# Optimization experiments

Measured on AMD Instinct MI355X. Metric: run time of the kernel, lower is better.

## Reference

```python
import jax, jax.numpy as jnp
import numpy as np

DIM_V = 512
H = 8
EPS = 1e-5

def _layernorm(x, g, b):
    mu = jnp.mean(x, axis=-1, keepdims=True)
    var = jnp.var(x, axis=-1, keepdims=True)
    return (x - mu) * jax.lax.rsqrt(var + EPS) * g + b

def setup_inputs() -> dict:
    key = jax.random.key(0)
    ks = jax.random.split(key, 10)
    B, Nq, Nk, dq, dk, dv = 8, 1024, 1024, 512, 512, DIM_V
    def lin(k, fan_in, shape):
        bound = 1.0 / np.sqrt(fan_in)
        return jax.random.uniform(k, shape, jnp.float32, -bound, bound)
    return {
        "Q": jax.random.normal(ks[0], (B, Nq, dq), jnp.float32),
        "K": jax.random.normal(ks[1], (B, Nk, dk), jnp.float32),
        "Wq": lin(ks[2], dq, (dv, dq)), "bq": lin(ks[3], dq, (dv,)),
        "Wk": lin(ks[4], dk, (dv, dk)), "bk": lin(ks[5], dk, (dv,)),
        "Wv": lin(ks[6], dk, (dv, dk)), "bv": lin(ks[7], dk, (dv,)),
        "Wo": lin(ks[8], dv, (dv, dv)), "bo": lin(ks[9], dv, (dv,)),
        "g0": jnp.ones((dv,), jnp.float32), "beta0": jnp.zeros((dv,), jnp.float32),
        "g1": jnp.ones((dv,), jnp.float32), "beta1": jnp.zeros((dv,), jnp.float32),
    }

def reference(Q, K, Wq, bq, Wk, bk, Wv, bv, Wo, bo, g0, beta0, g1, beta1):
    B, Nq, _ = Q.shape
    Nk = K.shape[1]
    d_h = DIM_V // H
    Qp = Q @ Wq.T + bq            # [B,Nq,dv]
    Kp = K @ Wk.T + bk            # [B,Nk,dv]
    Vp = K @ Wv.T + bv            # [B,Nk,dv]
    # split heads along feature dim (matches torch split(dim_split,2)+cat(0))
    Qh = Qp.reshape(B, Nq, H, d_h).transpose(0, 2, 1, 3)  # [B,H,Nq,dh]
    Kh = Kp.reshape(B, Nk, H, d_h).transpose(0, 2, 1, 3)
    Vh = Vp.reshape(B, Nk, H, d_h).transpose(0, 2, 1, 3)
    # NOTE: original scales by sqrt(dim_V), the FULL model dim
    scores = jnp.einsum('bhnd,bhmd->bhnm', Qh, Kh) / jnp.sqrt(jnp.float32(DIM_V))
    A = jax.nn.softmax(scores, axis=-1)                   # [B,H,Nq,Nk]
    Oh = Qh + jnp.einsum('bhnm,bhmd->bhnd', A, Vh)        # residual on projected Q
    O = Oh.transpose(0, 2, 1, 3).reshape(B, Nq, DIM_V)
    O = _layernorm(O, g0, beta0)
    O = O + jax.nn.relu(O @ Wo.T + bo)
    O = _layernorm(O, g1, beta1)
    return O
```

## Files before the change

### kernel.cpp

```cpp
#include <hip/hip_runtime.h>
#include <hip/hip_bf16.h>

typedef __hip_bfloat16 bf16;
typedef short bf16x8 __attribute__((ext_vector_type(8)));
typedef float f32x4 __attribute__((ext_vector_type(4)));
typedef unsigned int u32;

static __device__ __forceinline__ float bfu2f(unsigned short u) { return __uint_as_float((u32)u << 16); }
static __device__ __forceinline__ u32 pack2(float a, float b) {
    return (u32)__bfloat16_as_ushort(__float2bfloat16(a))
         | ((u32)__bfloat16_as_ushort(__float2bfloat16(b)) << 16);
}
static __device__ __forceinline__ float wave_sum(float v) {
    #pragma unroll
    for (int off = 32; off > 0; off >>= 1) v += __shfl_xor(v, off);
    return v;
}

static __device__ __forceinline__ void gll16(const bf16* g, bf16* l) {
    __builtin_amdgcn_global_load_lds((const __attribute__((address_space(1))) void*)g,
                                     (__attribute__((address_space(3))) void*)l,
                                     16, 0, 0);
}

__global__ __launch_bounds__(256) void castall(const float* __restrict__ Q,  const float* __restrict__ K,
                                               const float* __restrict__ Wq, const float* __restrict__ Wk,
                                               const float* __restrict__ Wv, const float* __restrict__ Wo,
                                               bf16* __restrict__ dQ,  bf16* __restrict__ dK,
                                               bf16* __restrict__ dWq, bf16* __restrict__ dWk,
                                               bf16* __restrict__ dWv, bf16* __restrict__ dWo)
{
    const int b = blockIdx.x;
    const float* src; bf16* dst; size_t off;
    if (b < 1024)      { src = Q;  dst = dQ;  off = (size_t)b * 4096; }
    else if (b < 2048) { src = K;  dst = dK;  off = (size_t)(b - 1024) * 4096; }
    else {
        const int wb = b - 2048, wi = wb >> 6;
        off = (size_t)(wb & 63) * 4096;
        src = wi == 0 ? Wq : wi == 1 ? Wk : wi == 2 ? Wv : Wo;
        dst = wi == 0 ? dWq : wi == 1 ? dWk : wi == 2 ? dWv : dWo;
    }
    const size_t p = off + threadIdx.x * 16;
    const float4 v0 = *(const float4*)(src + p);
    const float4 v1 = *(const float4*)(src + p + 4);
    const float4 v2 = *(const float4*)(src + p + 8);
    const float4 v3 = *(const float4*)(src + p + 12);
    uint4 o0, o1;
    o0.x = pack2(v0.x, v0.y); o0.y = pack2(v0.z, v0.w);
    o0.z = pack2(v1.x, v1.y); o0.w = pack2(v1.z, v1.w);
    o1.x = pack2(v2.x, v2.y); o1.y = pack2(v2.z, v2.w);
    o1.z = pack2(v3.x, v3.y); o1.w = pack2(v3.z, v3.w);
    *(uint4*)(dst + p)     = o0;
    *(uint4*)(dst + p + 8) = o1;
}

__global__ __launch_bounds__(256) void gemm_qkv(const bf16* __restrict__ Aq, const bf16* __restrict__ Ak,
                                                const bf16* __restrict__ Wq, const bf16* __restrict__ Wk,
                                                const bf16* __restrict__ Wv,
                                                const float* __restrict__ bq, const float* __restrict__ bk,
                                                const float* __restrict__ bv,
                                                bf16* __restrict__ oQ, bf16* __restrict__ oK,
                                                bf16* __restrict__ oV)
{
    __shared__ bf16 Xs[128 * 64];
    __shared__ bf16 Ws[128 * 64];

    const int tid = threadIdx.x, lane = tid & 63, wave = tid >> 6;
    const int yy = blockIdx.y, wi = yy >> 2;
    const bf16* A     = wi == 0 ? Aq : Ak;
    const bf16* W     = wi == 0 ? Wq : wi == 1 ? Wk : Wv;
    const float* bias = wi == 0 ? bq : wi == 1 ? bk : bv;
    bf16* out         = wi == 0 ? oQ : wi == 1 ? oK : oV;
    const bool vmode  = (wi == 2);
    const int bm = blockIdx.x * 128;
    const int bn = (yy & 3) * 128;

    const int srow = tid >> 3;
    const int sg8  = (((tid & 7) ^ (srow & 7)) * 8);
    const int wm = (wave >> 1) * 64, wn = (wave & 1) * 64;
    const int fr = lane & 15, fq = lane >> 4;

    f32x4 acc[4][4] = {};
    const bf16* Ap = A + (size_t)(bm + srow) * 512 + sg8;
    const bf16* Wp = W + (size_t)(bn + srow) * 512 + sg8;
    const int ld = 8 * tid;

    for (int k0 = 0; k0 < 512; k0 += 64) {
        __syncthreads();
        #pragma unroll
        for (int c = 0; c < 4; c++) {
            gll16(Ap + k0 + (size_t)(32 * c) * 512, Xs + ld + 2048 * c);
            gll16(Wp + k0 + (size_t)(32 * c) * 512, Ws + ld + 2048 * c);
        }
        __syncthreads();

        #pragma unroll
        for (int c2 = 0; c2 < 2; c2++) {
            bf16x8 fx[4], fw[4];
            #pragma unroll
            for (int i = 0; i < 4; i++) {
                const int rx = wm + 16 * i + fr;
                const int rw = wn + 16 * i + fr;
                fx[i] = *(const bf16x8*)(&Xs[rx * 64 + (((c2 * 4 + fq) ^ (rx & 7)) * 8)]);
                fw[i] = *(const bf16x8*)(&Ws[rw * 64 + (((c2 * 4 + fq) ^ (rw & 7)) * 8)]);
            }
            if (vmode) {
                #pragma unroll
                for (int i = 0; i < 4; i++)
                    #pragma unroll
                    for (int j = 0; j < 4; j++)
                        acc[i][j] = __builtin_amdgcn_mfma_f32_16x16x32_bf16(fx[i], fw[j], acc[i][j], 0, 0, 0);
            } else {
                #pragma unroll
                for (int i = 0; i < 4; i++)
                    #pragma unroll
                    for (int j = 0; j < 4; j++)
                        acc[i][j] = __builtin_amdgcn_mfma_f32_16x16x32_bf16(fw[i], fx[j], acc[i][j], 0, 0, 0);
            }
        }
    }

    if (!vmode) {
        #pragma unroll
        for (int i = 0; i < 4; i++) {
            const int colb = bn + wn + 16 * i + 4 * fq;
            const float4 b4 = *(const float4*)(bias + colb);
            const int h = colb >> 6, d0 = colb & 63;
            #pragma unroll
            for (int j = 0; j < 4; j++) {
                const int n = bm + wm + 16 * j + fr;
                const int b = n >> 10, nn = n & 1023;
                uint2 pk;
                pk.x = pack2(acc[i][j][0] + b4.x, acc[i][j][1] + b4.y);
                pk.y = pack2(acc[i][j][2] + b4.z, acc[i][j][3] + b4.w);
                *(uint2*)(out + ((size_t)(b * 8 + h) * 1024 + nn) * 64 + d0) = pk;
            }
        }
    } else {
        #pragma unroll
        for (int i = 0; i < 4; i++) {
            const int n0 = bm + wm + 16 * i + 4 * fq;
            const int b = n0 >> 10, nn = n0 & 1023;
            #pragma unroll
            for (int j = 0; j < 4; j++) {
                const int col = bn + wn + 16 * j + fr;
                const float bv2 = bias[col];
                const int h = col >> 6, d = col & 63;
                uint2 pk;
                pk.x = pack2(acc[i][j][0] + bv2, acc[i][j][1] + bv2);
                pk.y = pack2(acc[i][j][2] + bv2, acc[i][j][3] + bv2);
                *(uint2*)(out + ((size_t)(b * 8 + h) * 64 + d) * 1024 + nn) = pk;
            }
        }
    }
}

__global__ __launch_bounds__(256) void attn_mfma(const bf16* __restrict__ Qh,
                                                 const bf16* __restrict__ Kh,
                                                 const bf16* __restrict__ VhT,
                                                 bf16* __restrict__ Oc)
{
    __shared__ bf16 Ks[64 * 64];
    __shared__ bf16 Vs[64 * 64];
    __shared__ bf16 Ps[4][16 * 72];

    const int tid = threadIdx.x, lane = tid & 63, w = tid >> 6;
    const int id = blockIdx.x;
    const int bh = (id & 7) * 8 + (id >> 7);
    const int wq = ((id >> 3) & 15) * 64 + w * 16;

    const bf16* Qb = Qh  + ((size_t)bh * 1024 + wq) * 64;
    const bf16* Kb = Kh  + (size_t)bh * 1024 * 64;
    const bf16* Vb = VhT + (size_t)bh * 64 * 1024;

    const int fl = lane & 15, fq = lane >> 4;
    const int flk = fl & 7;
    const int gA = (fq ^ flk) * 8;
    const int gB = ((4 | fq) ^ flk) * 8;

    bf16x8 qf[2];
    qf[0] = *(const bf16x8*)(Qb + fl * 64 + fq * 8);
    qf[1] = *(const bf16x8*)(Qb + fl * 64 + 32 + fq * 8);

    f32x4 o[4] = {};
    float lsum = 0.f;
    const float sc2 = 0.04419417382415922f * 1.4426950408889634f;

    const int srow = tid >> 3;
    const int sg8  = (((tid & 7) ^ (srow & 7)) * 8);
    const bf16* KbR  = Kb + (size_t)srow * 64 + sg8;
    const bf16* VbR0 = Vb + (size_t)srow * 1024 + sg8;
    const bf16* VbR1 = Vb + (size_t)(srow + 32) * 1024 + sg8;
    const int ld = 8 * tid;

    for (int kt = 0; kt < 16; kt++) {
        const int m0 = kt * 64;
        __syncthreads();
        gll16(KbR + (size_t)m0 * 64,        Ks + ld);
        gll16(KbR + (size_t)(m0 + 32) * 64, Ks + 2048 + ld);
        gll16(VbR0 + m0,                    Vs + ld);
        gll16(VbR1 + m0,                    Vs + 2048 + ld);
        __syncthreads();

        bf16x8 kf[4][2];
        #pragma unroll
        for (int tm = 0; tm < 4; tm++) {
            kf[tm][0] = *(const bf16x8*)(&Ks[(16 * tm + fl) * 64 + gA]);
            kf[tm][1] = *(const bf16x8*)(&Ks[(16 * tm + fl) * 64 + gB]);
        }

        f32x4 st[4] = {};
        #pragma unroll
        for (int tm = 0; tm < 4; tm++) {
            st[tm] = __builtin_amdgcn_mfma_f32_16x16x32_bf16(kf[tm][0], qf[0], st[tm], 0, 0, 0);
            st[tm] = __builtin_amdgcn_mfma_f32_16x16x32_bf16(kf[tm][1], qf[1], st[tm], 0, 0, 0);
        }
        #pragma unroll
        for (int tm = 0; tm < 4; tm++) {
            float p0 = __builtin_amdgcn_exp2f(st[tm][0] * sc2);
            float p1 = __builtin_amdgcn_exp2f(st[tm][1] * sc2);
            float p2 = __builtin_amdgcn_exp2f(st[tm][2] * sc2);
            float p3 = __builtin_amdgcn_exp2f(st[tm][3] * sc2);
            lsum += (p0 + p1) + (p2 + p3);
            uint2 pk;
            pk.x = pack2(p0, p1);
            pk.y = pack2(p2, p3);
            *(uint2*)(&Ps[w][fl * 72 + 16 * tm + fq * 4]) = pk;
        }

        bf16x8 vf[4][2];
        #pragma unroll
        for (int jd = 0; jd < 4; jd++) {
            vf[jd][0] = *(const bf16x8*)(&Vs[(16 * jd + fl) * 64 + gA]);
            vf[jd][1] = *(const bf16x8*)(&Vs[(16 * jd + fl) * 64 + gB]);
        }
        bf16x8 pf0 = *(const bf16x8*)(&Ps[w][fl * 72 + fq * 8]);
        bf16x8 pf1 = *(const bf16x8*)(&Ps[w][fl * 72 + 32 + fq * 8]);
        #pragma unroll
        for (int jd = 0; jd < 4; jd++) {
            o[jd] = __builtin_amdgcn_mfma_f32_16x16x32_bf16(vf[jd][0], pf0, o[jd], 0, 0, 0);
            o[jd] = __builtin_amdgcn_mfma_f32_16x16x32_bf16(vf[jd][1], pf1, o[jd], 0, 0, 0);
        }
    }

    const int b = bh >> 3, h = bh & 7;
    float ls = lsum;
    ls += __shfl_xor(ls, 16);
    ls += __shfl_xor(ls, 32);
    const float linv = 1.f / ls;
    const size_t obase = ((size_t)(b * 1024 + wq + fl)) * 512 + h * 64;
    #pragma unroll
    for (int jd = 0; jd < 4; jd++) {
        const ushort4 qr = *(const ushort4*)(Qb + fl * 64 + 16 * jd + fq * 4);
        uint2 w2;
        w2.x = pack2(o[jd][0] * linv + bfu2f(qr.x), o[jd][1] * linv + bfu2f(qr.y));
        w2.y = pack2(o[jd][2] * linv + bfu2f(qr.z), o[jd][3] * linv + bfu2f(qr.w));
        *(uint2*)(&Oc[obase + 16 * jd + fq * 4]) = w2;
    }
}

__global__ __launch_bounds__(256) void ln0(const bf16* __restrict__ X,
                                           const float* __restrict__ g,
                                           const float* __restrict__ be,
                                           bf16* __restrict__ Y)
{
    const int lane = threadIdx.x & 63;
    const int row = blockIdx.x * 4 + (threadIdx.x >> 6);
    const size_t base = (size_t)row * 512 + lane * 8;
    const bf16x8 xv = *(const bf16x8*)(X + base);
    float x[8];
    #pragma unroll
    for (int j = 0; j < 8; j++) x[j] = bfu2f((unsigned short)xv[j]);
    float s = 0.f, s2 = 0.f;
    #pragma unroll
    for (int j = 0; j < 8; j++) { s += x[j]; s2 += x[j] * x[j]; }
    s = wave_sum(s); s2 = wave_sum(s2);
    const float mean = s * (1.f / 512.f);
    const float var = s2 * (1.f / 512.f) - mean * mean;
    const float rs = rsqrtf(fmaxf(var, 0.f) + 1e-5f);
    const float4 gv0 = *(const float4*)(g + lane * 8);
    const float4 gv1 = *(const float4*)(g + lane * 8 + 4);
    const float4 bv0 = *(const float4*)(be + lane * 8);
    const float4 bv1 = *(const float4*)(be + lane * 8 + 4);
    uint4 ov;
    ov.x = pack2((x[0]-mean)*rs*gv0.x + bv0.x, (x[1]-mean)*rs*gv0.y + bv0.y);
    ov.y = pack2((x[2]-mean)*rs*gv0.z + bv0.z, (x[3]-mean)*rs*gv0.w + bv0.w);
    ov.z = pack2((x[4]-mean)*rs*gv1.x + bv1.x, (x[5]-mean)*rs*gv1.y + bv1.y);
    ov.w = pack2((x[6]-mean)*rs*gv1.z + bv1.z, (x[7]-mean)*rs*gv1.w + bv1.w);
    *(uint4*)(Y + base) = ov;
}

__global__ __launch_bounds__(512) void gemm_fo_ln1(const bf16* __restrict__ A,
                                                   const bf16* __restrict__ W,
                                                   const float* __restrict__ bo,
                                                   const float* __restrict__ g1,
                                                   const float* __restrict__ be1,
                                                   float* __restrict__ out)
{
    __shared__ bf16 As[32 * 512];
    __shared__ bf16 Ws[512 * 64];
    __shared__ float2 red[32][8];

    const int tid = threadIdx.x, lane = tid & 63, w = tid >> 6;
    const int bm = blockIdx.x * 32;
    const int wn = w * 64;
    const int fr = lane & 15, fq = lane >> 4;

    const int ldb = 8 * tid;
    #pragma unroll
    for (int c = 0; c < 4; c++) {
        const int lin = tid + 512 * c;
        const int row = lin >> 6, g = lin & 63;
        gll16(A + (size_t)(bm + row) * 512 + ((g ^ (row & 7)) * 8),
              As + ldb + 4096 * c);
    }

    const int srow = tid >> 3;
    const int sg8  = (((tid & 7) ^ (srow & 7)) * 8);
    const bf16* Wp = W + (size_t)srow * 512 + sg8;

    f32x4 acc[4][2] = {};

    for (int kt = 0; kt < 8; kt++) {
        const int k0 = kt * 64;
        if (kt) __syncthreads();
        #pragma unroll
        for (int c = 0; c < 8; c++)
            gll16(Wp + k0 + (size_t)(64 * c) * 512, Ws + ldb + 4096 * c);
        __syncthreads();

        const int kb = kt * 8;
        #pragma unroll
        for (int c2 = 0; c2 < 2; c2++) {
            bf16x8 fx[2], fw[4];
            #pragma unroll
            for (int j = 0; j < 2; j++) {
                const int rx = 16 * j + fr;
                fx[j] = *(const bf16x8*)(&As[rx * 512 + (kb + ((c2 * 4 + fq) ^ (rx & 7))) * 8]);
            }
            #pragma unroll
            for (int i = 0; i < 4; i++) {
                const int rw = wn + 16 * i + fr;
                fw[i] = *(const bf16x8*)(&Ws[rw * 64 + (((c2 * 4 + fq) ^ (rw & 7)) * 8)]);
            }
            #pragma unroll
            for (int i = 0; i < 4; i++)
                #pragma unroll
                for (int j = 0; j < 2; j++)
                    acc[i][j] = __builtin_amdgcn_mfma_f32_16x16x32_bf16(fw[i], fx[j], acc[i][j], 0, 0, 0);
        }
    }

    float yv[4][2][4];
    float s[2] = {0.f, 0.f}, s2[2] = {0.f, 0.f};
    #pragma unroll
    for (int i = 0; i < 4; i++) {
        const int c = wn + 16 * i + 4 * fq;
        const float4 bo4 = *(const float4*)(bo + c);
        const int gc = c >> 3, co = c & 7;
        #pragma unroll
        for (int j = 0; j < 2; j++) {
            const int n = 16 * j + fr;
            const ushort4 rr = *(const ushort4*)(&As[n * 512 + ((gc ^ (n & 7)) * 8 + co)]);
            float y0 = bfu2f(rr.x) + fmaxf(acc[i][j][0] + bo4.x, 0.f);
            float y1 = bfu2f(rr.y) + fmaxf(acc[i][j][1] + bo4.y, 0.f);
            float y2 = bfu2f(rr.z) + fmaxf(acc[i][j][2] + bo4.z, 0.f);
            float y3 = bfu2f(rr.w) + fmaxf(acc[i][j][3] + bo4.w, 0.f);
            s[j]  += (y0 + y1) + (y2 + y3);
            s2[j] += (y0 * y0 + y1 * y1) + (y2 * y2 + y3 * y3);
            yv[i][j][0] = y0; yv[i][j][1] = y1; yv[i][j][2] = y2; yv[i][j][3] = y3;
        }
    }
    #pragma unroll
    for (int j = 0; j < 2; j++) {
        s[j]  += __shfl_xor(s[j], 16);  s[j]  += __shfl_xor(s[j], 32);
        s2[j] += __shfl_xor(s2[j], 16); s2[j] += __shfl_xor(s2[j], 32);
    }
    if (fq == 0) {
        red[fr][w]      = make_float2(s[0], s2[0]);
        red[16 + fr][w] = make_float2(s[1], s2[1]);
    }
    __syncthreads();
    float mu[2], rs[2];
    #pragma unroll
    for (int j = 0; j < 2; j++) {
        const int n = 16 * j + fr;
        float S = 0.f, S2 = 0.f;
        #pragma unroll
        for (int q = 0; q < 8; q++) { const float2 v = red[n][q]; S += v.x; S2 += v.y; }
        mu[j] = S * (1.f / 512.f);
        const float var = S2 * (1.f / 512.f) - mu[j] * mu[j];
        rs[j] = rsqrtf(fmaxf(var, 0.f) + 1e-5f);
    }
    #pragma unroll
    for (int i = 0; i < 4; i++) {
        const int c = wn + 16 * i + 4 * fq;
        const float4 g4 = *(const float4*)(g1 + c);
        const float4 b4 = *(const float4*)(be1 + c);
        #pragma unroll
        for (int j = 0; j < 2; j++) {
            const int n = bm + 16 * j + fr;
            float4 o4;
            o4.x = (yv[i][j][0] - mu[j]) * rs[j] * g4.x + b4.x;
            o4.y = (yv[i][j][1] - mu[j]) * rs[j] * g4.y + b4.y;
            o4.z = (yv[i][j][2] - mu[j]) * rs[j] * g4.z + b4.z;
            o4.w = (yv[i][j][3] - mu[j]) * rs[j] * g4.w + b4.w;
            *(float4*)(out + (size_t)n * 512 + c) = o4;
        }
    }
}

extern "C" void kernel_launch(void* const* d_in, const int* in_sizes, int n_in,
                              void* d_out, int out_size, void* d_ws, size_t ws_size,
                              hipStream_t stream)
{
    const float* Q   = (const float*)d_in[0];
    const float* K   = (const float*)d_in[1];
    const float* Wq  = (const float*)d_in[2];
    const float* bq  = (const float*)d_in[3];
    const float* Wk  = (const float*)d_in[4];
    const float* bk  = (const float*)d_in[5];
    const float* Wv  = (const float*)d_in[6];
    const float* bv  = (const float*)d_in[7];
    const float* Wo  = (const float*)d_in[8];
    const float* bo  = (const float*)d_in[9];
    const float* g0  = (const float*)d_in[10];
    const float* be0 = (const float*)d_in[11];
    const float* g1  = (const float*)d_in[12];
    const float* be1 = (const float*)d_in[13];
    float* out = (float*)d_out;

    const size_t NQK = (size_t)8 * 1024 * 512;
    const size_t NW  = (size_t)512 * 512;
    bf16* ws   = (bf16*)d_ws;
    bf16* cQ   = ws;
    bf16* cK   = cQ + NQK;
    bf16* cWq  = cK + NQK;
    bf16* cWk  = cWq + NW;
    bf16* cWv  = cWk + NW;
    bf16* cWo  = cWv + NW;
    bf16* pQh  = cWo + NW;
    bf16* pKh  = pQh + NQK;
    bf16* pVhT = pKh + NQK;
    bf16* pOc  = (bf16*)d_out;
    bf16* pO1  = pKh;

    castall<<<2304, 256, 0, stream>>>(Q, K, Wq, Wk, Wv, Wo, cQ, cK, cWq, cWk, cWv, cWo);
    gemm_qkv<<<dim3(64, 12), 256, 0, stream>>>(cQ, cK, cWq, cWk, cWv, bq, bk, bv, pQh, pKh, pVhT);
    attn_mfma<<<1024, 256, 0, stream>>>(pQh, pKh, pVhT, pOc);
    ln0<<<2048, 256, 0, stream>>>(pOc, g0, be0, pO1);
    gemm_fo_ln1<<<256, 512, 0, stream>>>(pO1, cWo, bo, g1, be1, out);
}
```

Before: 186.3 us.

## Fuse fp32-to-bf16 casts into GEMM loaders and LayerNorm0 into output GEMM

Removes the standalone cast kernel. The QKV GEMM and the output GEMM now load fp32 inputs and weights directly, converting them to bf16 in registers before storing to LDS. It also removes the separate ln0 kernel by normalizing the 32-row A tile in shared memory at the start of gemm_fo_ln1. This saves two launches and the global round-trips of the bf16 copies. The cost is that direct global_load_lds is replaced by register-staged loads (double fp32 traffic per tile and no async LDS path), and the fp32 weight tiles are reread and converted by every block.

```diff
diff --git a/kernel.cpp b/kernel.cpp
--- a/kernel.cpp
+++ b/kernel.cpp
@@ -11,11 +11,6 @@
     return (u32)__bfloat16_as_ushort(__float2bfloat16(a))
          | ((u32)__bfloat16_as_ushort(__float2bfloat16(b)) << 16);
 }
-static __device__ __forceinline__ float wave_sum(float v) {
-    #pragma unroll
-    for (int off = 32; off > 0; off >>= 1) v += __shfl_xor(v, off);
-    return v;
-}
 
 static __device__ __forceinline__ void gll16(const bf16* g, bf16* l) {
     __builtin_amdgcn_global_load_lds((const __attribute__((address_space(1))) void*)g,
@@ -23,40 +18,9 @@
                                      16, 0, 0);
 }
 
-__global__ __launch_bounds__(256) void castall(const float* __restrict__ Q,  const float* __restrict__ K,
-                                               const float* __restrict__ Wq, const float* __restrict__ Wk,
-                                               const float* __restrict__ Wv, const float* __restrict__ Wo,
-                                               bf16* __restrict__ dQ,  bf16* __restrict__ dK,
-                                               bf16* __restrict__ dWq, bf16* __restrict__ dWk,
-                                               bf16* __restrict__ dWv, bf16* __restrict__ dWo)
-{
-    const int b = blockIdx.x;
-    const float* src; bf16* dst; size_t off;
-    if (b < 1024)      { src = Q;  dst = dQ;  off = (size_t)b * 4096; }
-    else if (b < 2048) { src = K;  dst = dK;  off = (size_t)(b - 1024) * 4096; }
-    else {
-        const int wb = b - 2048, wi = wb >> 6;
-        off = (size_t)(wb & 63) * 4096;
-        src = wi == 0 ? Wq : wi == 1 ? Wk : wi == 2 ? Wv : Wo;
-        dst = wi == 0 ? dWq : wi == 1 ? dWk : wi == 2 ? dWv : dWo;
-    }
-    const size_t p = off + threadIdx.x * 16;
-    const float4 v0 = *(const float4*)(src + p);
-    const float4 v1 = *(const float4*)(src + p + 4);
-    const float4 v2 = *(const float4*)(src + p + 8);
-    const float4 v3 = *(const float4*)(src + p + 12);
-    uint4 o0, o1;
-    o0.x = pack2(v0.x, v0.y); o0.y = pack2(v0.z, v0.w);
-    o0.z = pack2(v1.x, v1.y); o0.w = pack2(v1.z, v1.w);
-    o1.x = pack2(v2.x, v2.y); o1.y = pack2(v2.z, v2.w);
-    o1.z = pack2(v3.x, v3.y); o1.w = pack2(v3.z, v3.w);
-    *(uint4*)(dst + p)     = o0;
-    *(uint4*)(dst + p + 8) = o1;
-}
-
-__global__ __launch_bounds__(256) void gemm_qkv(const bf16* __restrict__ Aq, const bf16* __restrict__ Ak,
-                                                const bf16* __restrict__ Wq, const bf16* __restrict__ Wk,
-                                                const bf16* __restrict__ Wv,
+__global__ __launch_bounds__(256) void gemm_qkv(const float* __restrict__ Aq, const float* __restrict__ Ak,
+                                                const float* __restrict__ Wq, const float* __restrict__ Wk,
+                                                const float* __restrict__ Wv,
                                                 const float* __restrict__ bq, const float* __restrict__ bk,
                                                 const float* __restrict__ bv,
                                                 bf16* __restrict__ oQ, bf16* __restrict__ oK,
@@ -67,8 +31,8 @@
 
     const int tid = threadIdx.x, lane = tid & 63, wave = tid >> 6;
     const int yy = blockIdx.y, wi = yy >> 2;
-    const bf16* A     = wi == 0 ? Aq : Ak;
-    const bf16* W     = wi == 0 ? Wq : wi == 1 ? Wk : Wv;
+    const float* A    = wi == 0 ? Aq : Ak;
+    const float* W    = wi == 0 ? Wq : wi == 1 ? Wk : Wv;
     const float* bias = wi == 0 ? bq : wi == 1 ? bk : bv;
     bf16* out         = wi == 0 ? oQ : wi == 1 ? oK : oV;
     const bool vmode  = (wi == 2);
@@ -81,16 +45,32 @@
     const int fr = lane & 15, fq = lane >> 4;
 
     f32x4 acc[4][4] = {};
-    const bf16* Ap = A + (size_t)(bm + srow) * 512 + sg8;
-    const bf16* Wp = W + (size_t)(bn + srow) * 512 + sg8;
+    const float* Ap = A + (size_t)(bm + srow) * 512 + sg8;
+    const float* Wp = W + (size_t)(bn + srow) * 512 + sg8;
     const int ld = 8 * tid;
 
     for (int k0 = 0; k0 < 512; k0 += 64) {
         __syncthreads();
         #pragma unroll
-        for (int c = 0; c < 4; c++) {
-            gll16(Ap + k0 + (size_t)(32 * c) * 512, Xs + ld + 2048 * c);
-            gll16(Wp + k0 + (size_t)(32 * c) * 512, Ws + ld + 2048 * c);
+        for (int cb = 0; cb < 2; cb++) {
+            float4 ab[2][2], wb[2][2];
+            #pragma unroll
+            for (int c = 0; c < 2; c++) {
+                const float* ap = Ap + k0 + (size_t)(32 * (2 * cb + c)) * 512;
+                const float* wp = Wp + k0 + (size_t)(32 * (2 * cb + c)) * 512;
+                ab[c][0] = *(const float4*)(ap); ab[c][1] = *(const float4*)(ap + 4);
+                wb[c][0] = *(const float4*)(wp); wb[c][1] = *(const float4*)(wp + 4);
+            }
+            #pragma unroll
+            for (int c = 0; c < 2; c++) {
+                uint4 av, wv;
+                av.x = pack2(ab[c][0].x, ab[c][0].y); av.y = pack2(ab[c][0].z, ab[c][0].w);
+                av.z = pack2(ab[c][1].x, ab[c][1].y); av.w = pack2(ab[c][1].z, ab[c][1].w);
+                wv.x = pack2(wb[c][0].x, wb[c][0].y); wv.y = pack2(wb[c][0].z, wb[c][0].w);
+                wv.z = pack2(wb[c][1].x, wb[c][1].y); wv.w = pack2(wb[c][1].z, wb[c][1].w);
+                *(uint4*)(Xs + ld + 2048 * (2 * cb + c)) = av;
+                *(uint4*)(Ws + ld + 2048 * (2 * cb + c)) = wv;
+            }
         }
         __syncthreads();
 
@@ -259,39 +239,10 @@
     }
 }
 
-__global__ __launch_bounds__(256) void ln0(const bf16* __restrict__ X,
-                                           const float* __restrict__ g,
-                                           const float* __restrict__ be,
-                                           bf16* __restrict__ Y)
-{
-    const int lane = threadIdx.x & 63;
-    const int row = blockIdx.x * 4 + (threadIdx.x >> 6);
-    const size_t base = (size_t)row * 512 + lane * 8;
-    const bf16x8 xv = *(const bf16x8*)(X + base);
-    float x[8];
-    #pragma unroll
-    for (int j = 0; j < 8; j++) x[j] = bfu2f((unsigned short)xv[j]);
-    float s = 0.f, s2 = 0.f;
-    #pragma unroll
-    for (int j = 0; j < 8; j++) { s += x[j]; s2 += x[j] * x[j]; }
-    s = wave_sum(s); s2 = wave_sum(s2);
-    const float mean = s * (1.f / 512.f);
-    const float var = s2 * (1.f / 512.f) - mean * mean;
-    const float rs = rsqrtf(fmaxf(var, 0.f) + 1e-5f);
-    const float4 gv0 = *(const float4*)(g + lane * 8);
-    const float4 gv1 = *(const float4*)(g + lane * 8 + 4);
-    const float4 bv0 = *(const float4*)(be + lane * 8);
-    const float4 bv1 = *(const float4*)(be + lane * 8 + 4);
-    uint4 ov;
-    ov.x = pack2((x[0]-mean)*rs*gv0.x + bv0.x, (x[1]-mean)*rs*gv0.y + bv0.y);
-    ov.y = pack2((x[2]-mean)*rs*gv0.z + bv0.z, (x[3]-mean)*rs*gv0.w + bv0.w);
-    ov.z = pack2((x[4]-mean)*rs*gv1.x + bv1.x, (x[5]-mean)*rs*gv1.y + bv1.y);
-    ov.w = pack2((x[6]-mean)*rs*gv1.z + bv1.z, (x[7]-mean)*rs*gv1.w + bv1.w);
-    *(uint4*)(Y + base) = ov;
-}
-
 __global__ __launch_bounds__(512) void gemm_fo_ln1(const bf16* __restrict__ A,
-                                                   const bf16* __restrict__ W,
+                                                   const float* __restrict__ Wo,
+                                                   const float* __restrict__ g0,
+                                                   const float* __restrict__ be0,
                                                    const float* __restrict__ bo,
                                                    const float* __restrict__ g1,
                                                    const float* __restrict__ be1,
@@ -314,10 +265,51 @@
         gll16(A + (size_t)(bm + row) * 512 + ((g ^ (row & 7)) * 8),
               As + ldb + 4096 * c);
     }
+    __syncthreads();
+
+    {
+        const int r = tid >> 4, ci = tid & 15;
+        const int lrow = r * 512;
+        const int rx = (r & 7) * 8;
+        float xv[4][8];
+        float s = 0.f, s2 = 0.f;
+        #pragma unroll
+        for (int gg = 0; gg < 4; gg++) {
+            const int g = ci * 4 + gg;
+            const bf16x8 v = *(const bf16x8*)(&As[lrow + ((g * 8) ^ rx)]);
+            #pragma unroll
+            for (int e = 0; e < 8; e++) {
+                const float f = bfu2f((unsigned short)v[e]);
+                xv[gg][e] = f; s += f; s2 += f * f;
+            }
+        }
+        #pragma unroll
+        for (int off = 1; off < 16; off <<= 1) {
+            s += __shfl_xor(s, off); s2 += __shfl_xor(s2, off);
+        }
+        const float mu  = s * (1.f / 512.f);
+        const float var = s2 * (1.f / 512.f) - mu * mu;
+        const float rs0 = rsqrtf(fmaxf(var, 0.f) + 1e-5f);
+        #pragma unroll
+        for (int gg = 0; gg < 4; gg++) {
+            const int g = ci * 4 + gg;
+            const float4 gv0 = *(const float4*)(g0 + g * 8);
+            const float4 gv1 = *(const float4*)(g0 + g * 8 + 4);
+            const float4 bv0 = *(const float4*)(be0 + g * 8);
+            const float4 bv1 = *(const float4*)(be0 + g * 8 + 4);
+            uint4 ov;
+            ov.x = pack2((xv[gg][0]-mu)*rs0*gv0.x + bv0.x, (xv[gg][1]-mu)*rs0*gv0.y + bv0.y);
+            ov.y = pack2((xv[gg][2]-mu)*rs0*gv0.z + bv0.z, (xv[gg][3]-mu)*rs0*gv0.w + bv0.w);
+            ov.z = pack2((xv[gg][4]-mu)*rs0*gv1.x + bv1.x, (xv[gg][5]-mu)*rs0*gv1.y + bv1.y);
+            ov.w = pack2((xv[gg][6]-mu)*rs0*gv1.z + bv1.z, (xv[gg][7]-mu)*rs0*gv1.w + bv1.w);
+            *(uint4*)(&As[lrow + ((g * 8) ^ rx)]) = ov;
+        }
+    }
+    __syncthreads();
 
     const int srow = tid >> 3;
     const int sg8  = (((tid & 7) ^ (srow & 7)) * 8);
-    const bf16* Wp = W + (size_t)srow * 512 + sg8;
+    const float* Wp = Wo + (size_t)srow * 512 + sg8;
 
     f32x4 acc[4][2] = {};
 
@@ -325,8 +317,21 @@
         const int k0 = kt * 64;
         if (kt) __syncthreads();
         #pragma unroll
-        for (int c = 0; c < 8; c++)
-            gll16(Wp + k0 + (size_t)(64 * c) * 512, Ws + ldb + 4096 * c);
+        for (int cb = 0; cb < 2; cb++) {
+            float4 wb[4][2];
+            #pragma unroll
+            for (int c = 0; c < 4; c++) {
+                const float* wp = Wp + k0 + (size_t)(64 * (4 * cb + c)) * 512;
+                wb[c][0] = *(const float4*)(wp); wb[c][1] = *(const float4*)(wp + 4);
+            }
+            #pragma unroll
+            for (int c = 0; c < 4; c++) {
+                uint4 wv;
+                wv.x = pack2(wb[c][0].x, wb[c][0].y); wv.y = pack2(wb[c][0].z, wb[c][0].w);
+                wv.z = pack2(wb[c][1].x, wb[c][1].y); wv.w = pack2(wb[c][1].z, wb[c][1].w);
+                *(uint4*)(Ws + ldb + 4096 * (4 * cb + c)) = wv;
+            }
+        }
         __syncthreads();
 
         const int kb = kt * 8;
@@ -431,23 +436,13 @@
     float* out = (float*)d_out;
 
     const size_t NQK = (size_t)8 * 1024 * 512;
-    const size_t NW  = (size_t)512 * 512;
     bf16* ws   = (bf16*)d_ws;
-    bf16* cQ   = ws;
-    bf16* cK   = cQ + NQK;
-    bf16* cWq  = cK + NQK;
-    bf16* cWk  = cWq + NW;
-    bf16* cWv  = cWk + NW;
-    bf16* cWo  = cWv + NW;
-    bf16* pQh  = cWo + NW;
+    bf16* pQh  = ws;
     bf16* pKh  = pQh + NQK;
     bf16* pVhT = pKh + NQK;
-    bf16* pOc  = (bf16*)d_out;
-    bf16* pO1  = pKh;
-
-    castall<<<2304, 256, 0, stream>>>(Q, K, Wq, Wk, Wv, Wo, cQ, cK, cWq, cWk, cWv, cWo);
-    gemm_qkv<<<dim3(64, 12), 256, 0, stream>>>(cQ, cK, cWq, cWk, cWv, bq, bk, bv, pQh, pKh, pVhT);
+    bf16* pOc  = pVhT + NQK;
+
+    gemm_qkv<<<dim3(64, 12), 256, 0, stream>>>(Q, K, Wq, Wk, Wv, bq, bk, bv, pQh, pKh, pVhT);
     attn_mfma<<<1024, 256, 0, stream>>>(pQh, pKh, pVhT, pOc);
-    ln0<<<2048, 256, 0, stream>>>(pOc, g0, be0, pO1);
-    gemm_fo_ln1<<<256, 512, 0, stream>>>(pO1, cWo, bo, g1, be1, out);
-}
+    gemm_fo_ln1<<<256, 512, 0, stream>>>(pOc, Wo, g0, be0, bo, g1, be1, out);
+}
```

After: 184.5 us. Within noise of the previous version (-1.0%).
